# Performance work log

Measured on AMD Instinct MI355X. Metric: run time of the kernel, lower is better.

## Reference

```python
import jax, jax.numpy as jnp
import numpy as np


def setup_inputs() -> dict:
    key = jax.random.key(0)
    ks = jax.random.split(key, 8)
    B, S, V, E, H = 64, 128, 8000, 256, 512
    scale = 0.05
    return {
        "inputs": jax.random.randint(ks[0], (B, S), 0, V, dtype=jnp.int64),
        "embedding": jax.random.normal(ks[1], (V, E), dtype=jnp.float32) * scale,
        "W_ih": jax.random.normal(ks[2], (4 * H, E), dtype=jnp.float32) * scale,
        "W_hh": jax.random.normal(ks[3], (4 * H, H), dtype=jnp.float32) * scale,
        "b_ih": jax.random.normal(ks[4], (4 * H,), dtype=jnp.float32) * scale,
        "b_hh": jax.random.normal(ks[5], (4 * H,), dtype=jnp.float32) * scale,
        "W_cls": jax.random.normal(ks[6], (V, H), dtype=jnp.float32) * scale,
        "b_cls": jax.random.normal(ks[7], (V,), dtype=jnp.float32) * scale,
    }


def reference(inputs, embedding, W_ih, W_hh, b_ih, b_hh, W_cls, b_cls):
    B, S = inputs.shape
    H = W_hh.shape[1]
    x = embedding[inputs]  # (B, S, E)
    # batch the input-to-hidden GEMM across all timesteps
    x_gates = jnp.einsum('bse,ge->bsg', x, W_ih) + b_ih + b_hh  # (B, S, 4H)

    def step(carry, xg):
        h, c = carry
        gates = xg + h @ W_hh.T  # (B, 4H)
        i, f, g, o = jnp.split(gates, 4, axis=-1)  # PyTorch LSTMCell gate order
        i = jax.nn.sigmoid(i)
        f = jax.nn.sigmoid(f)
        g = jnp.tanh(g)
        o = jax.nn.sigmoid(o)
        c = f * c + i * g
        h = o * jnp.tanh(c)
        return (h, c), h

    h0 = jnp.zeros((B, H), dtype=x.dtype)
    c0 = jnp.zeros((B, H), dtype=x.dtype)
    _, hs = jax.lax.scan(step, (h0, c0), jnp.swapaxes(x_gates, 0, 1))  # hs: (S, B, H)
    hidden = jnp.swapaxes(hs, 0, 1)  # (B, S, H)
    logits = jnp.einsum('bsh,vh->bsv', hidden, W_cls) + b_cls  # (B, S, V)
    y = jnp.transpose(logits, (0, 2, 1))  # (B, V, S)
    return jax.nn.log_softmax(y, axis=1)
```

## Files before the change

### kernel.cpp

```cpp
#include <hip/hip_runtime.h>


using u16   = unsigned short;
using u32   = unsigned int;
using u16x4 = __attribute__((ext_vector_type(4))) u16;
using u16x8 = __attribute__((ext_vector_type(8))) u16;
using bf16x8 = __attribute__((ext_vector_type(8))) __bf16;
using f32x4 = __attribute__((ext_vector_type(4))) float;

#define NB   64
#define NS   128
#define NV   8000
#define NVP  8192
#define NE   256
#define NH   512
#define NG   2048
#define NBS  8192
#define OUT_BSTRIDE 1024000
#define XG_SSTRIDE  131072

__device__ inline u16 f2bf(float f) {
    unsigned x = __builtin_bit_cast(unsigned, f);
    unsigned r = (x + 0x7FFFu + ((x >> 16) & 1u)) >> 16;
    return (u16)r;
}
__device__ inline float bf2f(u16 x) {
    u32 u = ((u32)x) << 16;
    return __builtin_bit_cast(float, u);
}

__device__ inline bf16x8 ld_frag(const u16* p) {
    u16x8 v = *(const u16x8*)p;
    return __builtin_bit_cast(bf16x8, v);
}

__device__ inline u32 load_llc(const u32* p) {
    u32 v;
    asm volatile("global_load_dword %0, %1, off sc0 sc1\n\t"
                 "s_waitcnt vmcnt(0)"
                 : "=v"(v) : "v"(p) : "memory");
    return v;
}
__device__ inline f32x4 load_llc16(const void* p) {
    f32x4 v;
    asm volatile("global_load_dwordx4 %0, %1, off sc0 sc1\n\t"
                 "s_waitcnt vmcnt(0)"
                 : "=v"(v) : "v"(p) : "memory");
    return v;
}
__device__ inline void store_llc(u32* p, u32 v) {
    asm volatile("global_store_dword %0, %1, off sc0 sc1"
                 :: "v"(p), "v"(v) : "memory");
}
__device__ inline void prefetch16(f32x4& d, const float* p) {
    asm volatile("global_load_dwordx4 %0, %1, off"
                 : "=v"(d) : "v"(p) : "memory");
}

__device__ inline void gload_lds16(const u16* g, u16* l) {
    __builtin_amdgcn_global_load_lds(
        (const __attribute__((address_space(1))) unsigned int*)(const void*)g,
        (__attribute__((address_space(3))) unsigned int*)(void*)l,
        16, 0, 0);
}

__device__ inline void quad_transpose(float v[4], int p) {
    float tb[4];
    #pragma unroll
    for (int q2 = 0; q2 < 4; ++q2) tb[q2] = __shfl_xor(v[q2 ^ 2], 2);
    #pragma unroll
    for (int q2 = 0; q2 < 4; ++q2) v[q2] = (((q2 ^ p) & 2) ? tb[q2] : v[q2]);
    #pragma unroll
    for (int q2 = 0; q2 < 4; ++q2) tb[q2] = __shfl_xor(v[q2 ^ 1], 1);
    #pragma unroll
    for (int q2 = 0; q2 < 4; ++q2) v[q2] = (((q2 ^ p) & 1) ? tb[q2] : v[q2]);
}

__device__ inline float lstm_cell(const float v[4], float& c) {
    float i_ = 1.f / (1.f + __expf(-v[0]));
    float f_ = 1.f / (1.f + __expf(-v[1]));
    float e2 = __expf(2.f * v[2]);
    float g_ = 1.f - 2.f / (e2 + 1.f);
    float o_ = 1.f / (1.f + __expf(-v[3]));
    c = f_ * c + i_ * g_;
    float e2c = __expf(2.f * c);
    return o_ * (1.f - 2.f / (e2c + 1.f));
}

__global__ void cvt_all(const float* __restrict__ e,  const float* __restrict__ wi,
                        const float* __restrict__ wh, const float* __restrict__ wc,
                        u16* __restrict__ de,  u16* __restrict__ dwi,
                        u16* __restrict__ dwh, u16* __restrict__ dwc) {
    const int N0 = NV * NE / 8, N1 = NG * NE / 8, N2 = NG * NH / 8, N3 = NV * NH / 8;
    const int total = N0 + N1 + N2 + N3;
    for (int i = blockIdx.x * blockDim.x + threadIdx.x; i < total;
         i += gridDim.x * blockDim.x) {
        const float* s; u16* d; int j;
        if (i < N0)                { s = e;  d = de;  j = i; }
        else if (i < N0 + N1)      { s = wi; d = dwi; j = i - N0; }
        else if (i < N0 + N1 + N2) { s = wh; d = dwh; j = i - N0 - N1; }
        else                       { s = wc; d = dwc; j = i - N0 - N1 - N2; }
        const float4* s4 = (const float4*)s;
        float4 a = s4[2 * j], b = s4[2 * j + 1];
        u16x8 o;
        o[0] = f2bf(a.x); o[1] = f2bf(a.y); o[2] = f2bf(a.z); o[3] = f2bf(a.w);
        o[4] = f2bf(b.x); o[5] = f2bf(b.y); o[6] = f2bf(b.z); o[7] = f2bf(b.w);
        ((u16x8*)d)[j] = o;
    }
}

__global__ __launch_bounds__(256) void k1_xgates(
    const u16* __restrict__ Wih, const u16* __restrict__ emb,
    const int* __restrict__ toks,
    const float* __restrict__ bih, const float* __restrict__ bhh,
    float* __restrict__ xg)
{
    __shared__ u16x8 Al8[512];
    __shared__ u16x8 Bl8[512];
    u16* Al = (u16*)Al8;
    u16* Bl = (u16*)Bl8;

    const int t = threadIdx.x;
    const int lane = t & 63, w = t >> 6;
    const int wm = w >> 1, wn = w & 1;
    const int gtile = blockIdx.y * 128, mtile = blockIdx.x * 128;

    const int r0 = t >> 2, r1 = r0 + 64, q = t & 3;
    const int m0 = mtile + r0, m1 = mtile + r1;
    const int tok0 = toks[(m0 & 63) * NS + (m0 >> 6)];
    const int tok1 = toks[(m1 & 63) * NS + (m1 >> 6)];

    f32x4 acc[4][4];
    for (int i = 0; i < 4; ++i)
        for (int j = 0; j < 4; ++j) acc[i][j] = {0.f, 0.f, 0.f, 0.f};

    const int kc8 = (lane >> 4) * 8;
    for (int kk = 0; kk < 8; ++kk) {
        const int k0 = kk * 32;
        *(u16x8*)&Al[t * 8]         = *(const u16x8*)&Wih[(gtile + r0) * NE + k0 + q * 8];
        *(u16x8*)&Al[(t + 256) * 8] = *(const u16x8*)&Wih[(gtile + r1) * NE + k0 + q * 8];
        *(u16x8*)&Bl[t * 8]         = *(const u16x8*)&emb[tok0 * NE + k0 + q * 8];
        *(u16x8*)&Bl[(t + 256) * 8] = *(const u16x8*)&emb[tok1 * NE + k0 + q * 8];
        __syncthreads();
        bf16x8 af[4], bf[4];
        #pragma unroll
        for (int i = 0; i < 4; ++i) {
            af[i] = ld_frag(&Al[(wm * 64 + i * 16 + (lane & 15)) * 32 + kc8]);
            bf[i] = ld_frag(&Bl[(wn * 64 + i * 16 + (lane & 15)) * 32 + kc8]);
        }
        #pragma unroll
        for (int fi = 0; fi < 4; ++fi)
            #pragma unroll
            for (int fj = 0; fj < 4; ++fj)
                acc[fi][fj] = __builtin_amdgcn_mfma_f32_16x16x32_bf16(
                    af[fi], bf[fj], acc[fi][fj], 0, 0, 0);
        __syncthreads();
    }

    #pragma unroll
    for (int fi = 0; fi < 4; ++fi) {
        const int g0 = gtile + wm * 64 + fi * 16 + ((lane >> 4) << 2);
        const float4 v1 = *(const float4*)&bih[g0];
        const float4 v2 = *(const float4*)&bhh[g0];
        float badd[4] = {v1.x + v2.x, v1.y + v2.y, v1.z + v2.z, v1.w + v2.w};
        #pragma unroll
        for (int fj = 0; fj < 4; ++fj) {
            const int m = mtile + wn * 64 + fj * 16 + (lane & 15);
            const int b = m & 63, s = m >> 6;
            float* dst = &xg[s * XG_SSTRIDE + b];
            #pragma unroll
            for (int r = 0; r < 4; ++r)
                dst[(g0 + r) * 64] = acc[fi][fj][r] + badd[r];
        }
    }
}

#define LSTM_NBLK 64

__global__ __launch_bounds__(512, 2) void k2_lstm(
    const u16* __restrict__ Whh,
    const float* __restrict__ xg,
    u16* __restrict__ hbuf,
    u16* __restrict__ hidden,
    u32* __restrict__ flags)
{
    __shared__ __align__(16) u16 hl[16 * 528];

    const int t = threadIdx.x, lane = t & 63, w = t >> 6;
    const int bg = blockIdx.x >> 3, ug = blockIdx.x & 7;
    const int j = lane & 15;
    const int kc8 = (lane >> 4) * 8;

    const int ubase = ug * 64 + w * 8;
    const int grow0 = (j & 3) * 512 + ubase + (j >> 2);
    const int grow1 = grow0 + 4;

    bf16x8 bw0[16], bw1[16];
    #pragma unroll
    for (int kk = 0; kk < 16; ++kk) {
        bw0[kk] = ld_frag(&Whh[grow0 * NH + kk * 32 + kc8]);
        bw1[kk] = ld_frag(&Whh[grow1 * NH + kk * 32 + kc8]);
    }
    #pragma unroll
    for (int kk = 0; kk < 16; ++kk) {
        f32x4 w0 = __builtin_bit_cast(f32x4, bw0[kk]);
        f32x4 w1 = __builtin_bit_cast(f32x4, bw1[kk]);
        asm volatile("" : "+v"(w0), "+v"(w1));
        bw0[kk] = __builtin_bit_cast(bf16x8, w0);
        bw1[kk] = __builtin_bit_cast(bf16x8, w1);
    }

    {
        u16x8 z = {0, 0, 0, 0, 0, 0, 0, 0};
        *(u16x8*)&hl[(8 + (t >> 6)) * 528 + (t & 63) * 8] = z;
    }

    const int srow = t >> 6, scol = (t & 63) * 8;
    const int soff = (bg * 8 + srow) * NH + scol;
    u16* hl_w = &hl[srow * 528 + scol];

    const int p = lane & 3;
    const int q = (lane >> 2) & 3;
    const int batg = bg * 8 + (lane >> 4) * 4 + p;
    const int un0 = ubase + q;
    const bool act = lane < 32;
    const bool sl = act && ((lane & 4) == 0);

    const int xoff0 = grow0 * 64 + bg * 8 + (lane >> 4) * 4;
    const int xoff1 = grow1 * 64 + bg * 8 + (lane >> 4) * 4;

    f32x4 xv0 = {0, 0, 0, 0}, xv1 = {0, 0, 0, 0};
    f32x4 xn0 = {0, 0, 0, 0}, xn1 = {0, 0, 0, 0};
    if (act) {
        xv0 = *(const f32x4*)&xg[xoff0];
        xv1 = *(const f32x4*)&xg[xoff1];
    }
    float cA = 0.f, cB = 0.f;

    for (int step = 0; step < NS; ++step) {
        if (act && step + 1 < NS) {
            const float* xb = &xg[(step + 1) * XG_SSTRIDE];
            prefetch16(xn0, &xb[xoff0]);
            prefetch16(xn1, &xb[xoff1]);
        }
        if (step > 0 && lane < 8) {
            const u32* fp = &flags[(bg * 8 + lane) * 32];
            while ((int)load_llc(fp) < step) __builtin_amdgcn_s_sleep(1);
        }
        {
            f32x4 hv = load_llc16(&hbuf[(step & 1) * (NB * NH) + soff]);
            *(f32x4*)hl_w = hv;
        }
        __syncthreads();

        f32x4 a00 = {0, 0, 0, 0}, a01 = {0, 0, 0, 0};
        f32x4 a10 = {0, 0, 0, 0}, a11 = {0, 0, 0, 0};
        #pragma unroll
        for (int kk = 0; kk < 16; ++kk) {
            bf16x8 av = *(const bf16x8*)&hl[j * 528 + kk * 32 + kc8];
            if (kk & 1) {
                a01 = __builtin_amdgcn_mfma_f32_16x16x32_bf16(av, bw0[kk], a01, 0, 0, 0);
                a11 = __builtin_amdgcn_mfma_f32_16x16x32_bf16(av, bw1[kk], a11, 0, 0, 0);
            } else {
                a00 = __builtin_amdgcn_mfma_f32_16x16x32_bf16(av, bw0[kk], a00, 0, 0, 0);
                a10 = __builtin_amdgcn_mfma_f32_16x16x32_bf16(av, bw1[kk], a10, 0, 0, 0);
            }
        }

        float v0[4], v1[4];
        #pragma unroll
        for (int r = 0; r < 4; ++r) {
            v0[r] = a00[r] + a01[r] + xv0[r];
            v1[r] = a10[r] + a11[r] + xv1[r];
        }
        quad_transpose(v0, p);
        quad_transpose(v1, p);

        float h0 = lstm_cell(v0, cA);
        float h1 = lstm_cell(v1, cB);
        u32 hb0 = f2bf(h0), hb1 = f2bf(h1);
        u32 o0 = (u32)__shfl_xor((int)hb0, 4);
        u32 o1 = (u32)__shfl_xor((int)hb1, 4);
        u32 pr0 = hb0 | (o0 << 16);
        u32 pr1 = hb1 | (o1 << 16);

        if (sl) {
            u16* hn = hbuf + ((step & 1) ^ 1) * (NB * NH);
            store_llc((u32*)&hn[batg * NH + un0], pr0);
            store_llc((u32*)&hn[batg * NH + un0 + 4], pr1);
        }
        xv0 = xn0; xv1 = xn1;
        __syncthreads();

        if (step + 1 < NS && t == 0)
            store_llc(&flags[blockIdx.x * 32], (u32)(step + 1));

        if (sl) {
            *(u32*)&hidden[(batg * NS + step) * NH + un0] = pr0;
            *(u32*)&hidden[(batg * NS + step) * NH + un0 + 4] = pr1;
        }
    }
}

template <bool PACK16>
__global__ __launch_bounds__(256) void k3_cls(
    const u16* __restrict__ Wc, const u16* __restrict__ hid,
    const float* __restrict__ bcls,
    float* __restrict__ outf, u16* __restrict__ outb,
    float* __restrict__ lse)
{
    __shared__ __align__(16) u16 Al[2][128 * 32];
    __shared__ __align__(16) u16 Bl[2][128 * 32];
    __shared__ float red[2][128];

    const int t = threadIdx.x;
    const int lane = t & 63, w = t >> 6;
    const int wm = w >> 1, wn = w & 1;
    const int vtile = blockIdx.y * 128, mtile = blockIdx.x * 128;

    const int srow = w * 16 + (lane >> 2);
    const int scol = (lane & 3) * 8;
    const u16* gA = &Wc[(vtile + srow) * NH + scol];
    const u16* gB = &hid[(mtile + srow) * NH + scol];
    const int lo0 = (w * 16) * 32;
    const int lo1 = (w * 16 + 64) * 32;

    f32x4 acc[4][4];
    for (int i = 0; i < 4; ++i)
        for (int j2 = 0; j2 < 4; ++j2) acc[i][j2] = {0.f, 0.f, 0.f, 0.f};

    const int kc8 = (lane >> 4) * 8;

    {
        gload_lds16(gA,           &Al[0][lo0]);
        gload_lds16(gA + 64 * NH, &Al[0][lo1]);
        gload_lds16(gB,           &Bl[0][lo0]);
        gload_lds16(gB + 64 * NH, &Bl[0][lo1]);
        asm volatile("s_waitcnt vmcnt(0)" ::: "memory");
        __syncthreads();
    }

    int cur = 0;
    for (int kk = 0; kk < 16; ++kk) {
        if (kk + 1 < 16) {
            const int k0 = (kk + 1) * 32;
            gload_lds16(gA + k0,           &Al[cur ^ 1][lo0]);
            gload_lds16(gA + 64 * NH + k0, &Al[cur ^ 1][lo1]);
            gload_lds16(gB + k0,           &Bl[cur ^ 1][lo0]);
            gload_lds16(gB + 64 * NH + k0, &Bl[cur ^ 1][lo1]);
        }
        bf16x8 mf[4], vf[4];
        #pragma unroll
        for (int i = 0; i < 4; ++i) {
            mf[i] = ld_frag(&Bl[cur][(wm * 64 + i * 16 + (lane & 15)) * 32 + kc8]);
            vf[i] = ld_frag(&Al[cur][(wn * 64 + i * 16 + (lane & 15)) * 32 + kc8]);
        }
        #pragma unroll
        for (int fi = 0; fi < 4; ++fi)
            #pragma unroll
            for (int fj = 0; fj < 4; ++fj)
                acc[fi][fj] = __builtin_amdgcn_mfma_f32_16x16x32_bf16(
                    mf[fi], vf[fj], acc[fi][fj], 0, 0, 0);
        asm volatile("s_waitcnt vmcnt(0)" ::: "memory");
        __syncthreads();
        cur ^= 1;
    }

    float lsum[4][4];
    #pragma unroll
    for (int fi = 0; fi < 4; ++fi)
        #pragma unroll
        for (int r = 0; r < 4; ++r) lsum[fi][r] = 0.f;

    #pragma unroll
    for (int fj = 0; fj < 4; ++fj) {
        const int v = vtile + wn * 64 + fj * 16 + (lane & 15);
        const bool vok = (v < NV);
        const float bc = vok ? bcls[v] : 0.f;
        #pragma unroll
        for (int fi = 0; fi < 4; ++fi) {
            const int m = mtile + wm * 64 + fi * 16 + ((lane >> 4) << 2);
            const int b = m >> 7, s = m & 127;
            float lg[4];
            #pragma unroll
            for (int r = 0; r < 4; ++r) {
                lg[r] = acc[fi][fj][r] + bc;
                if (vok) lsum[fi][r] += __expf(lg[r]);
            }
            if (vok) {
                if (PACK16) {
                    u16x4 o = {f2bf(lg[0]), f2bf(lg[1]), f2bf(lg[2]), f2bf(lg[3])};
                    *(u16x4*)&outb[b * OUT_BSTRIDE + v * NS + s] = o;
                } else {
                    float4 o = {lg[0], lg[1], lg[2], lg[3]};
                    *(float4*)&outf[b * OUT_BSTRIDE + v * NS + s] = o;
                }
            }
        }
    }

    #pragma unroll
    for (int fi = 0; fi < 4; ++fi)
        #pragma unroll
        for (int r = 0; r < 4; ++r) {
            float sv = lsum[fi][r];
            sv += __shfl_xor(sv, 1);
            sv += __shfl_xor(sv, 2);
            sv += __shfl_xor(sv, 4);
            sv += __shfl_xor(sv, 8);
            lsum[fi][r] = sv;
        }
    if ((lane & 15) == 0) {
        #pragma unroll
        for (int fi = 0; fi < 4; ++fi)
            #pragma unroll
            for (int r = 0; r < 4; ++r)
                red[wn][wm * 64 + fi * 16 + ((lane >> 4) << 2) + r] = lsum[fi][r];
    }
    __syncthreads();
    if (t < 128) {
        const int m = mtile + t;
        atomicAdd(&lse[m], red[0][t] + red[1][t]);
    }
}

__global__ void k4_log(const float* __restrict__ lse, float* __restrict__ ll) {
    int i = blockIdx.x * 256 + threadIdx.x;
    if (i < NBS) ll[i] = logf(lse[i]);
}

__global__ void k5_norm(float* __restrict__ out, const float* __restrict__ ll) {
    const int total4 = NB * NV * NS / 4;
    float4* o4 = (float4*)out;
    for (int i = blockIdx.x * blockDim.x + threadIdx.x; i < total4;
         i += gridDim.x * blockDim.x) {
        const int i4 = i * 4;
        const int b = i4 / OUT_BSTRIDE;
        const int s = i4 & 127;
        float4 v = o4[i];
        const float4 l = *(const float4*)&ll[b * NS + s];
        v.x -= l.x; v.y -= l.y; v.z -= l.z; v.w -= l.w;
        o4[i] = v;
    }
}

__global__ void k5_bf16(float* __restrict__ out, const u16* __restrict__ lgb,
                        const float* __restrict__ ll) {
    const int total4 = NB * NV * NS / 4;
    float4* o4 = (float4*)out;
    const u16x4* l4 = (const u16x4*)lgb;
    for (int i = blockIdx.x * blockDim.x + threadIdx.x; i < total4;
         i += gridDim.x * blockDim.x) {
        const int i4 = i * 4;
        const int b = i4 / OUT_BSTRIDE;
        const int s = i4 & 127;
        u16x4 g = l4[i];
        const float4 l = *(const float4*)&ll[b * NS + s];
        float4 v;
        v.x = bf2f(g[0]) - l.x;
        v.y = bf2f(g[1]) - l.y;
        v.z = bf2f(g[2]) - l.z;
        v.w = bf2f(g[3]) - l.w;
        o4[i] = v;
    }
}

extern "C" void kernel_launch(void* const* d_in, const int* in_sizes, int n_in,
                              void* d_out, int out_size, void* d_ws, size_t ws_size,
                              hipStream_t stream) {
    const int*   toks   = (const int*)d_in[0];
    const float* emb_f  = (const float*)d_in[1];
    const float* Wih_f  = (const float*)d_in[2];
    const float* Whh_f  = (const float*)d_in[3];
    const float* bih    = (const float*)d_in[4];
    const float* bhh    = (const float*)d_in[5];
    const float* Wcls_f = (const float*)d_in[6];
    const float* bcls   = (const float*)d_in[7];
    float* out = (float*)d_out;
    char*  ws  = (char*)d_ws;

    u32*   flags  = (u32*)(ws + 0);
    float* lse    = (float*)(ws + 8192);
    float* loglse = (float*)(ws + 40960);
    u16*   hbuf   = (u16*)(ws + 73728);
    u16*   embb   = (u16*)(ws + 204800);
    u16*   wihb   = (u16*)(ws + 4300800);
    u16*   whhb   = (u16*)(ws + 5349376);
    u16*   wclsb  = (u16*)(ws + 7446528);
    u16*   hidden = (u16*)(ws + 15835136);
    u16*   lgb    = (u16*)(ws + 24223744);
    const bool bigws = ws_size >= (size_t)24223744 + (size_t)NB * NV * NS * 2;

    float* xg = out;

    hipMemsetAsync(ws, 0, 204800, stream);
    hipMemsetAsync((char*)wclsb + NV * NH * 2, 0, (NVP - NV) * NH * 2, stream);

    cvt_all<<<2048, 256, 0, stream>>>(emb_f, Wih_f, Whh_f, Wcls_f,
                                      embb, wihb, whhb, wclsb);

    k1_xgates<<<dim3(64, 16), 256, 0, stream>>>(wihb, embb, toks, bih, bhh, xg);
    k2_lstm<<<LSTM_NBLK, 512, 0, stream>>>(whhb, xg, hbuf, hidden, flags);
    if (bigws) {
        k3_cls<true><<<dim3(64, 64), 256, 0, stream>>>(wclsb, hidden, bcls,
                                                       out, lgb, lse);
        k4_log<<<32, 256, 0, stream>>>(lse, loglse);
        k5_bf16<<<2048, 256, 0, stream>>>(out, lgb, loglse);
    } else {
        k3_cls<false><<<dim3(64, 64), 256, 0, stream>>>(wclsb, hidden, bcls,
                                                        out, lgb, lse);
        k4_log<<<32, 256, 0, stream>>>(lse, loglse);
        k5_norm<<<2048, 256, 0, stream>>>(out, loglse);
    }
}
```

Before: 600.1 us.

## Fuse LSTM recurrence with classifier GEMM via flag-driven overlap of timestep tiles

```diff
diff --git a/kernel.cpp b/kernel.cpp
--- a/kernel.cpp
+++ b/kernel.cpp
@@ -176,272 +176,284 @@
 }
 
 #define LSTM_NBLK 64
-
-__global__ __launch_bounds__(512, 2) void k2_lstm(
+#define CLS_NBLK  192
+#define NTILES    4096
+
+template <bool STORE_LOGITS>
+__global__ __launch_bounds__(512, 2) void k23_fused(
     const u16* __restrict__ Whh,
     const float* __restrict__ xg,
     u16* __restrict__ hbuf,
     u16* __restrict__ hidden,
-    u32* __restrict__ flags)
+    u32* __restrict__ flags,
+    const u16* __restrict__ Wc,
+    const float* __restrict__ bcls,
+    u16* __restrict__ lgb,
+    float* __restrict__ lse)
 {
     __shared__ __align__(16) u16 hl[16 * 528];
+    __shared__ __align__(16) u16 Al[2][4096];
+    __shared__ __align__(16) u16 Bl[2][4096];
+    __shared__ float red[2][128];
 
     const int t = threadIdx.x, lane = t & 63, w = t >> 6;
-    const int bg = blockIdx.x >> 3, ug = blockIdx.x & 7;
-    const int j = lane & 15;
+
+    if (blockIdx.x < LSTM_NBLK) {
+        const int bg = blockIdx.x >> 3, ug = blockIdx.x & 7;
+        const int j = lane & 15;
+        const int kc8 = (lane >> 4) * 8;
+
+        const int ubase = ug * 64 + w * 8;
+        const int grow0 = (j & 3) * 512 + ubase + (j >> 2);
+        const int grow1 = grow0 + 4;
+
+        bf16x8 bw0[16], bw1[16];
+        #pragma unroll
+        for (int kk = 0; kk < 16; ++kk) {
+            bw0[kk] = ld_frag(&Whh[grow0 * NH + kk * 32 + kc8]);
+            bw1[kk] = ld_frag(&Whh[grow1 * NH + kk * 32 + kc8]);
+        }
+        #pragma unroll
+        for (int kk = 0; kk < 16; ++kk) {
+            f32x4 w0 = __builtin_bit_cast(f32x4, bw0[kk]);
+            f32x4 w1 = __builtin_bit_cast(f32x4, bw1[kk]);
+            asm volatile("" : "+v"(w0), "+v"(w1));
+            bw0[kk] = __builtin_bit_cast(bf16x8, w0);
+            bw1[kk] = __builtin_bit_cast(bf16x8, w1);
+        }
+
+        {
+            u16x8 z = {0, 0, 0, 0, 0, 0, 0, 0};
+            *(u16x8*)&hl[(8 + (t >> 6)) * 528 + (t & 63) * 8] = z;
+        }
+
+        const int srow = t >> 6, scol = (t & 63) * 8;
+        const int soff = (bg * 8 + srow) * NH + scol;
+        u16* hl_w = &hl[srow * 528 + scol];
+
+        const int p = lane & 3;
+        const int q = (lane >> 2) & 3;
+        const int batg = bg * 8 + (lane >> 4) * 4 + p;
+        const int un0 = ubase + q;
+        const bool act = lane < 32;
+        const bool sl = act && ((lane & 4) == 0);
+
+        const int xoff0 = grow0 * 64 + bg * 8 + (lane >> 4) * 4;
+        const int xoff1 = grow1 * 64 + bg * 8 + (lane >> 4) * 4;
+
+        f32x4 xv0 = {0, 0, 0, 0}, xv1 = {0, 0, 0, 0};
+        f32x4 xn0 = {0, 0, 0, 0}, xn1 = {0, 0, 0, 0};
+        if (act) {
+            xv0 = *(const f32x4*)&xg[xoff0];
+            xv1 = *(const f32x4*)&xg[xoff1];
+        }
+        float cA = 0.f, cB = 0.f;
+
+        for (int step = 0; step < NS; ++step) {
+            if (act && step + 1 < NS) {
+                const float* xb = &xg[(step + 1) * XG_SSTRIDE];
+                prefetch16(xn0, &xb[xoff0]);
+                prefetch16(xn1, &xb[xoff1]);
+            }
+            if (step > 0 && lane < 8) {
+                const u32* fp = &flags[(bg * 8 + lane) * 32];
+                while ((int)load_llc(fp) < step) __builtin_amdgcn_s_sleep(1);
+            }
+            {
+                f32x4 hv = load_llc16(&hbuf[(step & 1) * (NB * NH) + soff]);
+                *(f32x4*)hl_w = hv;
+            }
+            __syncthreads();
+
+            f32x4 a00 = {0, 0, 0, 0}, a01 = {0, 0, 0, 0};
+            f32x4 a10 = {0, 0, 0, 0}, a11 = {0, 0, 0, 0};
+            #pragma unroll
+            for (int kk = 0; kk < 16; ++kk) {
+                bf16x8 av = *(const bf16x8*)&hl[j * 528 + kk * 32 + kc8];
+                if (kk & 1) {
+                    a01 = __builtin_amdgcn_mfma_f32_16x16x32_bf16(av, bw0[kk], a01, 0, 0, 0);
+                    a11 = __builtin_amdgcn_mfma_f32_16x16x32_bf16(av, bw1[kk], a11, 0, 0, 0);
+                } else {
+                    a00 = __builtin_amdgcn_mfma_f32_16x16x32_bf16(av, bw0[kk], a00, 0, 0, 0);
+                    a10 = __builtin_amdgcn_mfma_f32_16x16x32_bf16(av, bw1[kk], a10, 0, 0, 0);
+                }
+            }
+
+            float v0[4], v1[4];
+            #pragma unroll
+            for (int r = 0; r < 4; ++r) {
+                v0[r] = a00[r] + a01[r] + xv0[r];
+                v1[r] = a10[r] + a11[r] + xv1[r];
+            }
+            quad_transpose(v0, p);
+            quad_transpose(v1, p);
+
+            float h0 = lstm_cell(v0, cA);
+            float h1 = lstm_cell(v1, cB);
+            u32 hb0 = f2bf(h0), hb1 = f2bf(h1);
+            u32 o0 = (u32)__shfl_xor((int)hb0, 4);
+            u32 o1 = (u32)__shfl_xor((int)hb1, 4);
+            u32 pr0 = hb0 | (o0 << 16);
+            u32 pr1 = hb1 | (o1 << 16);
+
+            if (sl) {
+                u16* hn = hbuf + ((step & 1) ^ 1) * (NB * NH);
+                store_llc((u32*)&hn[batg * NH + un0], pr0);
+                store_llc((u32*)&hn[batg * NH + un0 + 4], pr1);
+            }
+            xv0 = xn0; xv1 = xn1;
+            __syncthreads();
+
+            if (step + 1 < NS && t == 0)
+                store_llc(&flags[blockIdx.x * 32], (u32)(step + 1));
+
+            if (sl) {
+                store_llc((u32*)&hidden[(batg * NS + step) * NH + un0], pr0);
+                store_llc((u32*)&hidden[(batg * NS + step) * NH + un0 + 4], pr1);
+            }
+        }
+        asm volatile("s_waitcnt vmcnt(0)" ::: "memory");
+        __syncthreads();
+        if (t == 0)
+            store_llc(&flags[blockIdx.x * 32], 1000u);
+        return;
+    }
+
+    const int cid = blockIdx.x - LSTM_NBLK;
+    const int sw = w & 3;
+    const int srow = sw * 16 + (lane >> 2);
+    const int scol = (lane & 3) * 8;
     const int kc8 = (lane >> 4) * 8;
-
-    const int ubase = ug * 64 + w * 8;
-    const int grow0 = (j & 3) * 512 + ubase + (j >> 2);
-    const int grow1 = grow0 + 4;
-
-    bf16x8 bw0[16], bw1[16];
-    #pragma unroll
-    for (int kk = 0; kk < 16; ++kk) {
-        bw0[kk] = ld_frag(&Whh[grow0 * NH + kk * 32 + kc8]);
-        bw1[kk] = ld_frag(&Whh[grow1 * NH + kk * 32 + kc8]);
-    }
-    #pragma unroll
-    for (int kk = 0; kk < 16; ++kk) {
-        f32x4 w0 = __builtin_bit_cast(f32x4, bw0[kk]);
-        f32x4 w1 = __builtin_bit_cast(f32x4, bw1[kk]);
-        asm volatile("" : "+v"(w0), "+v"(w1));
-        bw0[kk] = __builtin_bit_cast(bf16x8, w0);
-        bw1[kk] = __builtin_bit_cast(bf16x8, w1);
-    }
-
-    {
-        u16x8 z = {0, 0, 0, 0, 0, 0, 0, 0};
-        *(u16x8*)&hl[(8 + (t >> 6)) * 528 + (t & 63) * 8] = z;
-    }
-
-    const int srow = t >> 6, scol = (t & 63) * 8;
-    const int soff = (bg * 8 + srow) * NH + scol;
-    u16* hl_w = &hl[srow * 528 + scol];
-
-    const int p = lane & 3;
-    const int q = (lane >> 2) & 3;
-    const int batg = bg * 8 + (lane >> 4) * 4 + p;
-    const int un0 = ubase + q;
-    const bool act = lane < 32;
-    const bool sl = act && ((lane & 4) == 0);
-
-    const int xoff0 = grow0 * 64 + bg * 8 + (lane >> 4) * 4;
-    const int xoff1 = grow1 * 64 + bg * 8 + (lane >> 4) * 4;
-
-    f32x4 xv0 = {0, 0, 0, 0}, xv1 = {0, 0, 0, 0};
-    f32x4 xn0 = {0, 0, 0, 0}, xn1 = {0, 0, 0, 0};
-    if (act) {
-        xv0 = *(const f32x4*)&xg[xoff0];
-        xv1 = *(const f32x4*)&xg[xoff1];
-    }
-    float cA = 0.f, cB = 0.f;
-
-    for (int step = 0; step < NS; ++step) {
-        if (act && step + 1 < NS) {
-            const float* xb = &xg[(step + 1) * XG_SSTRIDE];
-            prefetch16(xn0, &xb[xoff0]);
-            prefetch16(xn1, &xb[xoff1]);
-        }
-        if (step > 0 && lane < 8) {
-            const u32* fp = &flags[(bg * 8 + lane) * 32];
-            while ((int)load_llc(fp) < step) __builtin_amdgcn_s_sleep(1);
-        }
-        {
-            f32x4 hv = load_llc16(&hbuf[(step & 1) * (NB * NH) + soff]);
-            *(f32x4*)hl_w = hv;
-        }
-        __syncthreads();
-
-        f32x4 a00 = {0, 0, 0, 0}, a01 = {0, 0, 0, 0};
-        f32x4 a10 = {0, 0, 0, 0}, a11 = {0, 0, 0, 0};
-        #pragma unroll
+    const int wm = w >> 1, wn = w & 1;
+
+    for (int tile = cid; tile < NTILES; tile += CLS_NBLK) {
+        const int qd = tile >> 7;
+        const int bh = (tile >> 6) & 1;
+        const int vt = tile & 63;
+        const int vtile = vt * 128;
+        const int s0 = qd * 4;
+
+        if (w == 0) {
+            const int thr = s0 + 5;
+            const u32* fp = &flags[lane * 32];
+            while ((int)load_llc(fp) < thr) __builtin_amdgcn_s_sleep(32);
+        }
+        __syncthreads();
+
+        const u16* g0; const u16* g1;
+        u16* d0base; u16* d1base;
+        if (w < 4) {
+            g0 = &Wc[(vtile + srow) * NH + scol];
+            g1 = &Wc[(vtile + srow + 64) * NH + scol];
+            d0base = &Al[0][(sw * 16) * 32];
+            d1base = &Al[0][(sw * 16 + 64) * 32];
+        } else {
+            const int lr0 = srow, lr1 = srow + 64;
+            const int hr0 = (bh * 32 + (lr0 >> 2)) * NS + s0 + (lr0 & 3);
+            const int hr1 = (bh * 32 + (lr1 >> 2)) * NS + s0 + (lr1 & 3);
+            g0 = &hidden[hr0 * NH + scol];
+            g1 = &hidden[hr1 * NH + scol];
+            d0base = &Bl[0][(sw * 16) * 32];
+            d1base = &Bl[0][(sw * 16 + 64) * 32];
+        }
+
+        gload_lds16(g0, d0base);
+        gload_lds16(g1, d1base);
+        asm volatile("s_waitcnt vmcnt(0)" ::: "memory");
+        __syncthreads();
+
+        f32x4 acc[4][4];
+        #pragma unroll
+        for (int i = 0; i < 4; ++i)
+            #pragma unroll
+            for (int j2 = 0; j2 < 4; ++j2) acc[i][j2] = {0.f, 0.f, 0.f, 0.f};
+
+        int cur = 0;
         for (int kk = 0; kk < 16; ++kk) {
-            bf16x8 av = *(const bf16x8*)&hl[j * 528 + kk * 32 + kc8];
-            if (kk & 1) {
-                a01 = __builtin_amdgcn_mfma_f32_16x16x32_bf16(av, bw0[kk], a01, 0, 0, 0);
-                a11 = __builtin_amdgcn_mfma_f32_16x16x32_bf16(av, bw1[kk], a11, 0, 0, 0);
-            } else {
-                a00 = __builtin_amdgcn_mfma_f32_16x16x32_bf16(av, bw0[kk], a00, 0, 0, 0);
-                a10 = __builtin_amdgcn_mfma_f32_16x16x32_bf16(av, bw1[kk], a10, 0, 0, 0);
-            }
-        }
-
-        float v0[4], v1[4];
-        #pragma unroll
-        for (int r = 0; r < 4; ++r) {
-            v0[r] = a00[r] + a01[r] + xv0[r];
-            v1[r] = a10[r] + a11[r] + xv1[r];
-        }
-        quad_transpose(v0, p);
-        quad_transpose(v1, p);
-
-        float h0 = lstm_cell(v0, cA);
-        float h1 = lstm_cell(v1, cB);
-        u32 hb0 = f2bf(h0), hb1 = f2bf(h1);
-        u32 o0 = (u32)__shfl_xor((int)hb0, 4);
-        u32 o1 = (u32)__shfl_xor((int)hb1, 4);
-        u32 pr0 = hb0 | (o0 << 16);
-        u32 pr1 = hb1 | (o1 << 16);
-
-        if (sl) {
-            u16* hn = hbuf + ((step & 1) ^ 1) * (NB * NH);
-            store_llc((u32*)&hn[batg * NH + un0], pr0);
-            store_llc((u32*)&hn[batg * NH + un0 + 4], pr1);
-        }
-        xv0 = xn0; xv1 = xn1;
-        __syncthreads();
-
-        if (step + 1 < NS && t == 0)
-            store_llc(&flags[blockIdx.x * 32], (u32)(step + 1));
-
-        if (sl) {
-            *(u32*)&hidden[(batg * NS + step) * NH + un0] = pr0;
-            *(u32*)&hidden[(batg * NS + step) * NH + un0 + 4] = pr1;
-        }
-    }
-}
-
-template <bool PACK16>
-__global__ __launch_bounds__(256) void k3_cls(
-    const u16* __restrict__ Wc, const u16* __restrict__ hid,
-    const float* __restrict__ bcls,
-    float* __restrict__ outf, u16* __restrict__ outb,
-    float* __restrict__ lse)
-{
-    __shared__ __align__(16) u16 Al[2][128 * 32];
-    __shared__ __align__(16) u16 Bl[2][128 * 32];
-    __shared__ float red[2][128];
-
-    const int t = threadIdx.x;
-    const int lane = t & 63, w = t >> 6;
-    const int wm = w >> 1, wn = w & 1;
-    const int vtile = blockIdx.y * 128, mtile = blockIdx.x * 128;
-
-    const int srow = w * 16 + (lane >> 2);
-    const int scol = (lane & 3) * 8;
-    const u16* gA = &Wc[(vtile + srow) * NH + scol];
-    const u16* gB = &hid[(mtile + srow) * NH + scol];
-    const int lo0 = (w * 16) * 32;
-    const int lo1 = (w * 16 + 64) * 32;
-
-    f32x4 acc[4][4];
-    for (int i = 0; i < 4; ++i)
-        for (int j2 = 0; j2 < 4; ++j2) acc[i][j2] = {0.f, 0.f, 0.f, 0.f};
-
-    const int kc8 = (lane >> 4) * 8;
-
-    {
-        gload_lds16(gA,           &Al[0][lo0]);
-        gload_lds16(gA + 64 * NH, &Al[0][lo1]);
-        gload_lds16(gB,           &Bl[0][lo0]);
-        gload_lds16(gB + 64 * NH, &Bl[0][lo1]);
-        asm volatile("s_waitcnt vmcnt(0)" ::: "memory");
-        __syncthreads();
-    }
-
-    int cur = 0;
-    for (int kk = 0; kk < 16; ++kk) {
-        if (kk + 1 < 16) {
-            const int k0 = (kk + 1) * 32;
-            gload_lds16(gA + k0,           &Al[cur ^ 1][lo0]);
-            gload_lds16(gA + 64 * NH + k0, &Al[cur ^ 1][lo1]);
-            gload_lds16(gB + k0,           &Bl[cur ^ 1][lo0]);
-            gload_lds16(gB + 64 * NH + k0, &Bl[cur ^ 1][lo1]);
-        }
-        bf16x8 mf[4], vf[4];
-        #pragma unroll
-        for (int i = 0; i < 4; ++i) {
-            mf[i] = ld_frag(&Bl[cur][(wm * 64 + i * 16 + (lane & 15)) * 32 + kc8]);
-            vf[i] = ld_frag(&Al[cur][(wn * 64 + i * 16 + (lane & 15)) * 32 + kc8]);
-        }
-        #pragma unroll
-        for (int fi = 0; fi < 4; ++fi)
-            #pragma unroll
-            for (int fj = 0; fj < 4; ++fj)
-                acc[fi][fj] = __builtin_amdgcn_mfma_f32_16x16x32_bf16(
-                    mf[fi], vf[fj], acc[fi][fj], 0, 0, 0);
-        asm volatile("s_waitcnt vmcnt(0)" ::: "memory");
-        __syncthreads();
-        cur ^= 1;
-    }
-
-    float lsum[4][4];
-    #pragma unroll
-    for (int fi = 0; fi < 4; ++fi)
-        #pragma unroll
-        for (int r = 0; r < 4; ++r) lsum[fi][r] = 0.f;
-
-    #pragma unroll
-    for (int fj = 0; fj < 4; ++fj) {
-        const int v = vtile + wn * 64 + fj * 16 + (lane & 15);
-        const bool vok = (v < NV);
-        const float bc = vok ? bcls[v] : 0.f;
-        #pragma unroll
-        for (int fi = 0; fi < 4; ++fi) {
-            const int m = mtile + wm * 64 + fi * 16 + ((lane >> 4) << 2);
-            const int b = m >> 7, s = m & 127;
-            float lg[4];
-            #pragma unroll
-            for (int r = 0; r < 4; ++r) {
-                lg[r] = acc[fi][fj][r] + bc;
-                if (vok) lsum[fi][r] += __expf(lg[r]);
-            }
-            if (vok) {
-                if (PACK16) {
-                    u16x4 o = {f2bf(lg[0]), f2bf(lg[1]), f2bf(lg[2]), f2bf(lg[3])};
-                    *(u16x4*)&outb[b * OUT_BSTRIDE + v * NS + s] = o;
-                } else {
-                    float4 o = {lg[0], lg[1], lg[2], lg[3]};
-                    *(float4*)&outf[b * OUT_BSTRIDE + v * NS + s] = o;
+            if (kk + 1 < 16) {
+                const int k0 = (kk + 1) * 32;
+                const int boff = (cur ^ 1) * 4096;
+                gload_lds16(g0 + k0, d0base + boff);
+                gload_lds16(g1 + k0, d1base + boff);
+            }
+            if (w < 4) {
+                bf16x8 mf[4], vf[4];
+                #pragma unroll
+                for (int i = 0; i < 4; ++i) {
+                    mf[i] = ld_frag(&Bl[cur][(wm * 64 + i * 16 + (lane & 15)) * 32 + kc8]);
+                    vf[i] = ld_frag(&Al[cur][(wn * 64 + i * 16 + (lane & 15)) * 32 + kc8]);
                 }
-            }
-        }
-    }
-
-    #pragma unroll
-    for (int fi = 0; fi < 4; ++fi)
-        #pragma unroll
-        for (int r = 0; r < 4; ++r) {
-            float sv = lsum[fi][r];
-            sv += __shfl_xor(sv, 1);
-            sv += __shfl_xor(sv, 2);
-            sv += __shfl_xor(sv, 4);
-            sv += __shfl_xor(sv, 8);
-            lsum[fi][r] = sv;
-        }
-    if ((lane & 15) == 0) {
-        #pragma unroll
-        for (int fi = 0; fi < 4; ++fi)
-            #pragma unroll
-            for (int r = 0; r < 4; ++r)
-                red[wn][wm * 64 + fi * 16 + ((lane >> 4) << 2) + r] = lsum[fi][r];
-    }
-    __syncthreads();
-    if (t < 128) {
-        const int m = mtile + t;
-        atomicAdd(&lse[m], red[0][t] + red[1][t]);
+                #pragma unroll
+                for (int fi = 0; fi < 4; ++fi)
+                    #pragma unroll
+                    for (int fj = 0; fj < 4; ++fj)
+                        acc[fi][fj] = __builtin_amdgcn_mfma_f32_16x16x32_bf16(
+                            mf[fi], vf[fj], acc[fi][fj], 0, 0, 0);
+            }
+            asm volatile("s_waitcnt vmcnt(0)" ::: "memory");
+            __syncthreads();
+            cur ^= 1;
+        }
+
+        if (w < 4) {
+            float lsum[4][4];
+            #pragma unroll
+            for (int fi = 0; fi < 4; ++fi)
+                #pragma unroll
+                for (int r = 0; r < 4; ++r) lsum[fi][r] = 0.f;
+
+            #pragma unroll
+            for (int fj = 0; fj < 4; ++fj) {
+                const int v = vtile + wn * 64 + fj * 16 + (lane & 15);
+                const bool vok = (v < NV);
+                const float bc = vok ? bcls[v] : 0.f;
+                #pragma unroll
+                for (int fi = 0; fi < 4; ++fi) {
+                    const int lrb = wm * 64 + fi * 16 + ((lane >> 4) << 2);
+                    const int b = bh * 32 + (lrb >> 2);
+                    float lg[4];
+                    #pragma unroll
+                    for (int r = 0; r < 4; ++r) {
+                        lg[r] = acc[fi][fj][r] + bc;
+                        if (vok) lsum[fi][r] += __expf(lg[r]);
+                    }
+                    if (vok && STORE_LOGITS) {
+                        u16x4 o = {f2bf(lg[0]), f2bf(lg[1]), f2bf(lg[2]), f2bf(lg[3])};
+                        *(u16x4*)&lgb[b * OUT_BSTRIDE + v * NS + s0] = o;
+                    }
+                }
+            }
+
+            #pragma unroll
+            for (int fi = 0; fi < 4; ++fi)
+                #pragma unroll
+                for (int r = 0; r < 4; ++r) {
+                    float sv = lsum[fi][r];
+                    sv += __shfl_xor(sv, 1);
+                    sv += __shfl_xor(sv, 2);
+                    sv += __shfl_xor(sv, 4);
+                    sv += __shfl_xor(sv, 8);
+                    lsum[fi][r] = sv;
+                }
+            if ((lane & 15) == 0) {
+                #pragma unroll
+                for (int fi = 0; fi < 4; ++fi)
+                    #pragma unroll
+                    for (int r = 0; r < 4; ++r)
+                        red[wn][wm * 64 + fi * 16 + ((lane >> 4) << 2) + r] = lsum[fi][r];
+            }
+        }
+        __syncthreads();
+        if (t < 128) {
+            const int m = (bh * 32 + (t >> 2)) * NS + s0 + (t & 3);
+            atomicAdd(&lse[m], red[0][t] + red[1][t]);
+        }
     }
 }
 
 __global__ void k4_log(const float* __restrict__ lse, float* __restrict__ ll) {
     int i = blockIdx.x * 256 + threadIdx.x;
     if (i < NBS) ll[i] = logf(lse[i]);
-}
-
-__global__ void k5_norm(float* __restrict__ out, const float* __restrict__ ll) {
-    const int total4 = NB * NV * NS / 4;
-    float4* o4 = (float4*)out;
-    for (int i = blockIdx.x * blockDim.x + threadIdx.x; i < total4;
-         i += gridDim.x * blockDim.x) {
-        const int i4 = i * 4;
-        const int b = i4 / OUT_BSTRIDE;
-        const int s = i4 & 127;
-        float4 v = o4[i];
-        const float4 l = *(const float4*)&ll[b * NS + s];
-        v.x -= l.x; v.y -= l.y; v.z -= l.z; v.w -= l.w;
-        o4[i] = v;
-    }
 }
 
 __global__ void k5_bf16(float* __restrict__ out, const u16* __restrict__ lgb,
@@ -465,6 +477,85 @@
     }
 }
 
+__global__ __launch_bounds__(256) void k3_final(
+    const u16* __restrict__ Wc, const u16* __restrict__ hid,
+    const float* __restrict__ bcls, const float* __restrict__ ll,
+    float* __restrict__ out)
+{
+    __shared__ __align__(16) u16 Al[2][4096];
+    __shared__ __align__(16) u16 Bl[2][4096];
+
+    const int t = threadIdx.x;
+    const int lane = t & 63, w = t >> 6;
+    const int wm = w >> 1, wn = w & 1;
+    const int vtile = blockIdx.y * 128, mtile = blockIdx.x * 128;
+
+    const int srow = w * 16 + (lane >> 2);
+    const int scol = (lane & 3) * 8;
+    const u16* gA = &Wc[(vtile + srow) * NH + scol];
+    const u16* gB = &hid[(mtile + srow) * NH + scol];
+    const int lo0 = (w * 16) * 32;
+    const int lo1 = (w * 16 + 64) * 32;
+
+    f32x4 acc[4][4];
+    for (int i = 0; i < 4; ++i)
+        for (int j2 = 0; j2 < 4; ++j2) acc[i][j2] = {0.f, 0.f, 0.f, 0.f};
+
+    const int kc8 = (lane >> 4) * 8;
+    {
+        gload_lds16(gA,           &Al[0][lo0]);
+        gload_lds16(gA + 64 * NH, &Al[0][lo1]);
+        gload_lds16(gB,           &Bl[0][lo0]);
+        gload_lds16(gB + 64 * NH, &Bl[0][lo1]);
+        asm volatile("s_waitcnt vmcnt(0)" ::: "memory");
+        __syncthreads();
+    }
+    int cur = 0;
+    for (int kk = 0; kk < 16; ++kk) {
+        if (kk + 1 < 16) {
+            const int k0 = (kk + 1) * 32;
+            gload_lds16(gA + k0,           &Al[cur ^ 1][lo0]);
+            gload_lds16(gA + 64 * NH + k0, &Al[cur ^ 1][lo1]);
+            gload_lds16(gB + k0,           &Bl[cur ^ 1][lo0]);
+            gload_lds16(gB + 64 * NH + k0, &Bl[cur ^ 1][lo1]);
+        }
+        bf16x8 mf[4], vf[4];
+        #pragma unroll
+        for (int i = 0; i < 4; ++i) {
+            mf[i] = ld_frag(&Bl[cur][(wm * 64 + i * 16 + (lane & 15)) * 32 + kc8]);
+            vf[i] = ld_frag(&Al[cur][(wn * 64 + i * 16 + (lane & 15)) * 32 + kc8]);
+        }
+        #pragma unroll
+        for (int fi = 0; fi < 4; ++fi)
+            #pragma unroll
+            for (int fj = 0; fj < 4; ++fj)
+                acc[fi][fj] = __builtin_amdgcn_mfma_f32_16x16x32_bf16(
+                    mf[fi], vf[fj], acc[fi][fj], 0, 0, 0);
+        asm volatile("s_waitcnt vmcnt(0)" ::: "memory");
+        __syncthreads();
+        cur ^= 1;
+    }
+
+    #pragma unroll
+    for (int fj = 0; fj < 4; ++fj) {
+        const int v = vtile + wn * 64 + fj * 16 + (lane & 15);
+        if (v >= NV) continue;
+        const float bc = bcls[v];
+        #pragma unroll
+        for (int fi = 0; fi < 4; ++fi) {
+            const int m = mtile + wm * 64 + fi * 16 + ((lane >> 4) << 2);
+            const int b = m >> 7, s = m & 127;
+            const float4 lv = *(const float4*)&ll[m];
+            float4 o;
+            o.x = acc[fi][fj][0] + bc - lv.x;
+            o.y = acc[fi][fj][1] + bc - lv.y;
+            o.z = acc[fi][fj][2] + bc - lv.z;
+            o.w = acc[fi][fj][3] + bc - lv.w;
+            *(float4*)&out[b * OUT_BSTRIDE + v * NS + s] = o;
+        }
+    }
+}
+
 extern "C" void kernel_launch(void* const* d_in, const int* in_sizes, int n_in,
                               void* d_out, int out_size, void* d_ws, size_t ws_size,
                               hipStream_t stream) {
@@ -500,16 +591,16 @@
                                       embb, wihb, whhb, wclsb);
 
     k1_xgates<<<dim3(64, 16), 256, 0, stream>>>(wihb, embb, toks, bih, bhh, xg);
-    k2_lstm<<<LSTM_NBLK, 512, 0, stream>>>(whhb, xg, hbuf, hidden, flags);
     if (bigws) {
-        k3_cls<true><<<dim3(64, 64), 256, 0, stream>>>(wclsb, hidden, bcls,
-                                                       out, lgb, lse);
+        k23_fused<true><<<LSTM_NBLK + CLS_NBLK, 512, 0, stream>>>(
+            whhb, xg, hbuf, hidden, flags, wclsb, bcls, lgb, lse);
         k4_log<<<32, 256, 0, stream>>>(lse, loglse);
         k5_bf16<<<2048, 256, 0, stream>>>(out, lgb, loglse);
     } else {
-        k3_cls<false><<<dim3(64, 64), 256, 0, stream>>>(wclsb, hidden, bcls,
-                                                        out, lgb, lse);
+        k23_fused<false><<<LSTM_NBLK + CLS_NBLK, 512, 0, stream>>>(
+            whhb, xg, hbuf, hidden, flags, wclsb, bcls, lgb, lse);
         k4_log<<<32, 256, 0, stream>>>(lse, loglse);
-        k5_norm<<<2048, 256, 0, stream>>>(out, loglse);
-    }
-}
+        k3_final<<<dim3(64, 64), 256, 0, stream>>>(wclsb, hidden, bcls,
+                                                   loglse, out);
+    }
+}
```

Result: slower. 673.7 us (+12.3%).
